# Optimization experiments

Measured on AMD Instinct MI355X. Metric: run time of the kernel, lower is better.

The kernel has to match this reference:

```python
import jax, jax.numpy as jnp
import numpy as np

D_EMBED = 512
NUM_HEADS = 8
HEAD_DIM = D_EMBED // NUM_HEADS
D_FF = 2048
B, L = 2, 4096
LN_EPS = 1e-5


def _layernorm(x, g, b):
    mu = jnp.mean(x, axis=-1, keepdims=True)
    var = jnp.mean(jnp.square(x - mu), axis=-1, keepdims=True)
    return (x - mu) * jax.lax.rsqrt(var + LN_EPS) * g + b


def setup_inputs() -> dict:
    key = jax.random.key(0)
    ks = jax.random.split(key, 16)
    s = 0.02
    inp = {
        "x": jax.random.normal(ks[0], (B, L, D_EMBED), dtype=jnp.float32),
        "mask": jnp.ones((B, 1, 1, L), dtype=jnp.int32),
        # attention projections (stored [in, out] for x @ W)
        "Wq": jax.random.normal(ks[1], (D_EMBED, D_EMBED), dtype=jnp.float32) * s,
        "bq": jnp.zeros((D_EMBED,), dtype=jnp.float32),
        "Wk": jax.random.normal(ks[2], (D_EMBED, D_EMBED), dtype=jnp.float32) * s,
        "bk": jnp.zeros((D_EMBED,), dtype=jnp.float32),
        "Wv": jax.random.normal(ks[3], (D_EMBED, D_EMBED), dtype=jnp.float32) * s,
        "bv": jnp.zeros((D_EMBED,), dtype=jnp.float32),
        "Wo": jax.random.normal(ks[4], (D_EMBED, D_EMBED), dtype=jnp.float32) * s,
        "bo": jnp.zeros((D_EMBED,), dtype=jnp.float32),
        # layernorms
        "ln1_g": jnp.ones((D_EMBED,), dtype=jnp.float32),
        "ln1_b": jnp.zeros((D_EMBED,), dtype=jnp.float32),
        "ln2_g": jnp.ones((D_EMBED,), dtype=jnp.float32),
        "ln2_b": jnp.zeros((D_EMBED,), dtype=jnp.float32),
        # FFN
        "W1": jax.random.normal(ks[5], (D_EMBED, D_FF), dtype=jnp.float32) * s,
        "b1": jnp.zeros((D_FF,), dtype=jnp.float32),
        "W2": jax.random.normal(ks[6], (D_FF, D_EMBED), dtype=jnp.float32) * s,
        "b2": jnp.zeros((D_EMBED,), dtype=jnp.float32),
    }
    return inp


def reference(x, mask, Wq, bq, Wk, bk, Wv, bv, Wo, bo, ln1_g, ln1_b,
              W1, b1, W2, b2, ln2_g, ln2_b):
    Bx, Lx, _ = x.shape
    # projections -> [B, H, L, Dh]
    def split_heads(t):
        return t.reshape(Bx, Lx, NUM_HEADS, HEAD_DIM).transpose(0, 2, 1, 3)
    q = split_heads(x @ Wq + bq)
    k = split_heads(x @ Wk + bk)
    v = split_heads(x @ Wv + bv)
    scores = jnp.einsum("bhqd,bhkd->bhqk", q, k) / jnp.sqrt(
        jnp.asarray(HEAD_DIM, dtype=x.dtype))
    scores = jnp.where(mask == 0, jnp.asarray(-1e9, dtype=x.dtype), scores)
    attn = jax.nn.softmax(scores, axis=-1)
    ctx = jnp.einsum("bhqk,bhkd->bhqd", attn, v)
    ctx = ctx.transpose(0, 2, 1, 3).reshape(Bx, Lx, D_EMBED)
    attn_out = ctx @ Wo + bo

    h = _layernorm(x + attn_out, ln1_g, ln1_b)
    ff = (jax.nn.gelu(h @ W1 + b1, approximate=False)) @ W2 + b2
    return _layernorm(h + ff, ln2_g, ln2_b)
```

## Files before the change

kernel.cpp:

```cpp
#include <hip/hip_runtime.h>
#include <hip/hip_bf16.h>
#include <math.h>

#define D_EMBED 512
#define NUM_HEADS 8
#define HEAD_DIM 64
#define D_FF 2048
#define BATCH 2
#define SEQ 4096
#define M_ROWS (BATCH*SEQ)
#define QSCALE 0.18033688011112042f

typedef __attribute__((ext_vector_type(8))) short short8;
typedef __attribute__((ext_vector_type(4))) short short4_t;
typedef __attribute__((ext_vector_type(4))) float f32x4;
typedef __attribute__((ext_vector_type(16))) float f32x16;

#if __has_builtin(__builtin_amdgcn_exp2f)
#define EXP2(x) __builtin_amdgcn_exp2f(x)
#else
#define EXP2(x) exp2f(x)
#endif

__device__ inline unsigned short f2b(float f) {
    union { float f; unsigned u; } v; v.f = f;
    unsigned r = v.u + 0x7fffu + ((v.u >> 16) & 1u);
    return (unsigned short)(r >> 16);
}

__device__ inline float b2f(short s) {
    union { unsigned u; float f; } v;
    v.u = ((unsigned)(unsigned short)s) << 16;
    return v.f;
}

__device__ inline short4_t pk4(float p0, float p1, float p2, float p3) {
    union { __hip_bfloat162 h2[2]; short4_t s4; } u;
    u.h2[0] = __float22bfloat162_rn(make_float2(p0, p1));
    u.h2[1] = __float22bfloat162_rn(make_float2(p2, p3));
    return u.s4;
}

__device__ inline unsigned pk2(float lo, float hi) {
    union { __hip_bfloat162 h2; unsigned u; } x;
    x.h2 = __float22bfloat162_rn(make_float2(lo, hi));
    return x.u;
}

__device__ inline void plswap(unsigned a, unsigned b, unsigned &r0, unsigned &r1) {
#if __has_builtin(__builtin_amdgcn_permlane32_swap)
    auto v = __builtin_amdgcn_permlane32_swap(a, b, false, false);
    r0 = (unsigned)v[0]; r1 = (unsigned)v[1];
#else
    unsigned ax = (unsigned)__shfl_xor((int)a, 32, 64);
    unsigned bx = (unsigned)__shfl_xor((int)b, 32, 64);
    bool hi = (threadIdx.x & 32) != 0;
    r0 = hi ? bx : a;
    r1 = hi ? b  : ax;
#endif
}

__device__ inline short8 pfrag8(const float* p) {
    unsigned a0 = pk2(p[0], p[1]), a1 = pk2(p[2], p[3]);
    unsigned b0 = pk2(p[4], p[5]), b1 = pk2(p[6], p[7]);
    unsigned u0, u1, u2, u3;
    plswap(a0, b0, u0, u1);
    plswap(a1, b1, u2, u3);
    union { unsigned u[4]; short8 s; } r;
    r.u[0] = u0; r.u[1] = u2; r.u[2] = u1; r.u[3] = u3;
    return r.s;
}

__device__ inline void gl2lds16(const void* g, void* l) {
    __builtin_amdgcn_global_load_lds(
        (const __attribute__((address_space(1))) unsigned int*)g,
        (__attribute__((address_space(3))) unsigned int*)l, 16, 0, 0);
}

template<int EPI>
__global__ __launch_bounds__(256) void gemm_bt(
    const unsigned short* __restrict__ A, const unsigned short* __restrict__ BT,
    const float* __restrict__ bias, void* __restrict__ Cout,
    int M, int N, int K)
{
    __shared__ __align__(16) unsigned short As[128*32];
    __shared__ __align__(16) unsigned short Bs[128*32];
    const int tid  = threadIdx.x;
    const int wave = tid >> 6, lane = tid & 63;
    const int wy = wave >> 1, wx = wave & 1;
    const int quad = lane >> 4, m16 = lane & 15;
    const int row0 = blockIdx.y * 128, n0 = blockIdx.x * 128;
    const int rdoff = (quad ^ ((m16 >> 1) & 3)) * 8;

    f32x4 acc[4][4];
#pragma unroll
    for (int i = 0; i < 4; i++)
#pragma unroll
        for (int j = 0; j < 4; j++) acc[i][j] = (f32x4){0.f,0.f,0.f,0.f};

    const int kIters = K >> 5;
    for (int kt = 0; kt < kIters; ++kt) {
        const int k0 = kt << 5;
#pragma unroll
        for (int it = 0; it < 2; ++it) {
            int g  = it*256 + tid;
            int r  = g >> 2;
            int c8 = (((g & 3) ^ ((g >> 3) & 3)) << 3);
            gl2lds16(A  + (size_t)(row0 + r)*K + k0 + c8, &As[(size_t)(it*256 + wave*64)*8]);
            gl2lds16(BT + (size_t)(n0  + r)*K + k0 + c8, &Bs[(size_t)(it*256 + wave*64)*8]);
        }
        __syncthreads();
        short8 a[4], b[4];
#pragma unroll
        for (int i = 0; i < 4; i++) a[i] = *(const short8*)&As[(wy*64 + i*16 + m16)*32 + rdoff];
#pragma unroll
        for (int j = 0; j < 4; j++) b[j] = *(const short8*)&Bs[(wx*64 + j*16 + m16)*32 + rdoff];
#pragma unroll
        for (int i = 0; i < 4; i++)
#pragma unroll
            for (int j = 0; j < 4; j++)
                acc[i][j] = __builtin_amdgcn_mfma_f32_16x16x32_bf16(a[i], b[j], acc[i][j], 0, 0, 0);
        __syncthreads();
    }

#pragma unroll
    for (int j = 0; j < 4; j++) {
        int col = n0 + wx*64 + j*16 + m16;
        float bj = bias[col];
#pragma unroll
        for (int i = 0; i < 4; i++) {
            int rbase = row0 + wy*64 + i*16 + quad*4;
#pragma unroll
            for (int r = 0; r < 4; r++) {
                float v = acc[i][j][r] + bj;
                size_t idx = (size_t)(rbase + r)*N + col;
                if (EPI == 0) {
                    ((unsigned short*)Cout)[idx] = f2b(v);
                } else {
                    float gv = 0.5f * v * (1.0f + erff(v * 0.70710678118654752f));
                    ((unsigned short*)Cout)[idx] = f2b(gv);
                }
            }
        }
    }
}

__global__ __launch_bounds__(256) void gemm_qkv(
    const unsigned short* __restrict__ A, const unsigned short* __restrict__ BT,
    const float* __restrict__ bias,
    unsigned short* __restrict__ Qp, unsigned short* __restrict__ Kp,
    unsigned short* __restrict__ Vp)
{
    const int K = 512;
    __shared__ __align__(16) unsigned short As[128*32];
    __shared__ __align__(16) unsigned short Bs[128*32];
    const int tid  = threadIdx.x;
    const int wave = tid >> 6, lane = tid & 63;
    const int wy = wave >> 1, wx = wave & 1;
    const int quad = lane >> 4, m16 = lane & 15;
    const int row0 = blockIdx.y * 128, n0 = blockIdx.x * 128;
    const int rdoff = (quad ^ ((m16 >> 1) & 3)) * 8;
    const int region = n0 >> 9;

    f32x4 acc[4][4];
#pragma unroll
    for (int i = 0; i < 4; i++)
#pragma unroll
        for (int j = 0; j < 4; j++) acc[i][j] = (f32x4){0.f,0.f,0.f,0.f};

    for (int kt = 0; kt < 16; ++kt) {
        const int k0 = kt << 5;
#pragma unroll
        for (int it = 0; it < 2; ++it) {
            int g  = it*256 + tid;
            int r  = g >> 2;
            int c8 = (((g & 3) ^ ((g >> 3) & 3)) << 3);
            gl2lds16(A  + (size_t)(row0 + r)*K + k0 + c8, &As[(size_t)(it*256 + wave*64)*8]);
            gl2lds16(BT + (size_t)(n0  + r)*K + k0 + c8, &Bs[(size_t)(it*256 + wave*64)*8]);
        }
        __syncthreads();
        short8 a[4], b[4];
#pragma unroll
        for (int i = 0; i < 4; i++) a[i] = *(const short8*)&As[(wy*64 + i*16 + m16)*32 + rdoff];
#pragma unroll
        for (int j = 0; j < 4; j++) b[j] = *(const short8*)&Bs[(wx*64 + j*16 + m16)*32 + rdoff];
#pragma unroll
        for (int i = 0; i < 4; i++)
#pragma unroll
            for (int j = 0; j < 4; j++)
                acc[i][j] = __builtin_amdgcn_mfma_f32_16x16x32_bf16(a[i], b[j], acc[i][j], 0, 0, 0);
        __syncthreads();
    }

    const float sc = (region == 0) ? QSCALE : 1.0f;
#pragma unroll
    for (int j = 0; j < 4; j++) {
        int col = n0 + wx*64 + j*16 + m16;
        float bj = bias[col];
        int cc = col & 511, h = cc >> 6, d = cc & 63;
#pragma unroll
        for (int i = 0; i < 4; i++) {
            int rbase = row0 + wy*64 + i*16 + quad*4;
#pragma unroll
            for (int r = 0; r < 4; r++) {
                float v = (acc[i][j][r] + bj) * sc;
                int row = rbase + r;
                int b = row >> 12, l = row & 4095;
                size_t bh = (size_t)(b*8 + h);
                if (region == 0) {
                    Qp[(bh*SEQ + l)*64 + d] = f2b(v);
                } else if (region == 1) {
                    Kp[(bh*SEQ + l)*64 + d] = f2b(v);
                } else {
                    Vp[(bh*64 + d)*SEQ + l] = f2b(v);
                }
            }
        }
    }
}

__global__ __launch_bounds__(256) void gemm_bt64(
    const unsigned short* __restrict__ A, const unsigned short* __restrict__ BT,
    const float* __restrict__ bias, unsigned short* __restrict__ Cout,
    int M, int N, int K)
{
    __shared__ __align__(16) unsigned short As[64*32];
    __shared__ __align__(16) unsigned short Bs[128*32];
    const int tid  = threadIdx.x;
    const int wave = tid >> 6, lane = tid & 63;
    const int wy = wave >> 1, wx = wave & 1;
    const int quad = lane >> 4, m16 = lane & 15;
    const int row0 = blockIdx.y * 64, n0 = blockIdx.x * 128;
    const int rdoff = (quad ^ ((m16 >> 1) & 3)) * 8;

    f32x4 acc[2][4];
#pragma unroll
    for (int i = 0; i < 2; i++)
#pragma unroll
        for (int j = 0; j < 4; j++) acc[i][j] = (f32x4){0.f,0.f,0.f,0.f};

    const int kIters = K >> 5;
    for (int kt = 0; kt < kIters; ++kt) {
        const int k0 = kt << 5;
        {
            int r = tid >> 2;
            int c8 = (((tid & 3) ^ ((tid >> 3) & 3)) << 3);
            gl2lds16(A + (size_t)(row0 + r)*K + k0 + c8, &As[(size_t)(wave*64)*8]);
        }
#pragma unroll
        for (int it = 0; it < 2; ++it) {
            int g  = it*256 + tid;
            int r  = g >> 2;
            int c8 = (((g & 3) ^ ((g >> 3) & 3)) << 3);
            gl2lds16(BT + (size_t)(n0 + r)*K + k0 + c8, &Bs[(size_t)(it*256 + wave*64)*8]);
        }
        __syncthreads();
        short8 a[2], b[4];
#pragma unroll
        for (int i = 0; i < 2; i++) a[i] = *(const short8*)&As[(wy*32 + i*16 + m16)*32 + rdoff];
#pragma unroll
        for (int j = 0; j < 4; j++) b[j] = *(const short8*)&Bs[(wx*64 + j*16 + m16)*32 + rdoff];
#pragma unroll
        for (int i = 0; i < 2; i++)
#pragma unroll
            for (int j = 0; j < 4; j++)
                acc[i][j] = __builtin_amdgcn_mfma_f32_16x16x32_bf16(a[i], b[j], acc[i][j], 0, 0, 0);
        __syncthreads();
    }

#pragma unroll
    for (int j = 0; j < 4; j++) {
        int col = n0 + wx*64 + j*16 + m16;
        float bj = bias[col];
#pragma unroll
        for (int i = 0; i < 2; i++) {
            int rbase = row0 + wy*32 + i*16 + quad*4;
#pragma unroll
            for (int r = 0; r < 4; r++) {
                float v = acc[i][j][r] + bj;
                Cout[(size_t)(rbase + r)*N + col] = f2b(v);
            }
        }
    }
}

__global__ __launch_bounds__(256) void prep(
    const float* __restrict__ Wq, const float* __restrict__ Wk,
    const float* __restrict__ Wv, const float* __restrict__ Wo,
    const float* __restrict__ W1, const float* __restrict__ W2,
    const float* __restrict__ bq, const float* __restrict__ bk,
    const float* __restrict__ bv, const int* __restrict__ mask,
    unsigned short* __restrict__ WqkvT, unsigned short* __restrict__ WoT,
    unsigned short* __restrict__ W1T, unsigned short* __restrict__ W2T,
    float* __restrict__ bqkv, int* __restrict__ mflag, unsigned* __restrict__ kmax2)
{
    const int id = blockIdx.x, t = threadIdx.x;
    if (id == 3072) {
        if (t < 64) {
            const int* m = mask + t*128;
            int all = 1;
            for (int i = 0; i < 128; i += 4) {
                int4 v = *(const int4*)(m + i);
                all &= (v.x && v.y && v.z && v.w) ? 1 : 0;
            }
            mflag[t] = all;
        }
        if (t < 16) kmax2[t] = 0u;
        for (int i = t; i < 1536; i += 256)
            bqkv[i] = (i < 512) ? bq[i] : ((i < 1024) ? bk[i-512] : bv[i-1024]);
        return;
    }
    __shared__ float tt[32][33];
    const float* W; unsigned short* WT; int K, N, bx, by;
    if (id < 256)       { W = Wq; WT = WqkvT;            K = 512;  N = 512;  bx = id & 15;  by = id >> 4; }
    else if (id < 512)  { int l = id - 256;  W = Wk; WT = WqkvT + 512*512;  K = 512;  N = 512;  bx = l & 15; by = l >> 4; }
    else if (id < 768)  { int l = id - 512;  W = Wv; WT = WqkvT + 1024*512; K = 512;  N = 512;  bx = l & 15; by = l >> 4; }
    else if (id < 1024) { int l = id - 768;  W = Wo; WT = WoT;              K = 512;  N = 512;  bx = l & 15; by = l >> 4; }
    else if (id < 2048) { int l = id - 1024; W = W1; WT = W1T;              K = 512;  N = 2048; bx = l & 63; by = l >> 6; }
    else                { int l = id - 2048; W = W2; WT = W2T;              K = 2048; N = 512;  bx = l & 15; by = l >> 4; }
    const int n0 = bx*32, k0 = by*32;
    const int x = t & 31, y = t >> 5;
#pragma unroll
    for (int yy = y; yy < 32; yy += 8) tt[yy][x] = W[(size_t)(k0+yy)*N + n0 + x];
    __syncthreads();
#pragma unroll
    for (int yy = y; yy < 32; yy += 8) WT[(size_t)(n0+yy)*K + k0 + x] = f2b(tt[x][yy]);
}

__global__ __launch_bounds__(256) void kmax_k(
    const unsigned short* __restrict__ Kp, unsigned* __restrict__ kmax2)
{
    const int bh = blockIdx.x, t = threadIdx.x;
    const int row = blockIdx.y*256 + t;
    const unsigned short* kp = Kp + ((size_t)bh*SEQ + row)*64;
    float s = 0.f;
#pragma unroll
    for (int c = 0; c < 8; ++c) {
        short8 v = *(const short8*)(kp + c*8);
#pragma unroll
        for (int j = 0; j < 8; ++j) { float f = b2f(v[j]); s += f*f; }
    }
#pragma unroll
    for (int off = 32; off >= 1; off >>= 1)
        s = fmaxf(s, __shfl_xor(s, off, 64));
    if ((t & 63) == 0) atomicMax(&kmax2[bh], __float_as_uint(s));
}

__global__ __launch_bounds__(256, 1) void flash_attn(
    const unsigned short* __restrict__ Qp, const unsigned short* __restrict__ Kp,
    const unsigned short* __restrict__ Vt, const int* __restrict__ mask,
    const int* __restrict__ flags, const unsigned* __restrict__ kmax2,
    unsigned short* __restrict__ O)
{
    __shared__ __align__(16) unsigned short Ks[2][128*64];
    __shared__ __align__(16) unsigned short Vs[2][64*128];
    const int tid = threadIdx.x, wave = tid >> 6, lane = tid & 63;
    const int c = lane & 31, l5 = lane >> 5;
    const int bh = blockIdx.y, b = bh >> 3, h = bh & 7;
    const int qbase = blockIdx.x * 256 + wave * 64;

    const unsigned short* Qb = Qp + (size_t)bh*SEQ*64;
    const unsigned short* Kb = Kp + (size_t)bh*SEQ*64;
    const unsigned short* Vb = Vt + (size_t)bh*64*SEQ;
    const int* mbase = mask + b*SEQ;
    const int* fbase = flags + b*(SEQ/128);
    const float kmx = __uint_as_float(kmax2[bh]);

    short8 qf[2][4];
    float Mq[2];
#pragma unroll
    for (int qs = 0; qs < 2; ++qs) {
        const unsigned short* qp = Qb + (size_t)(qbase + qs*32 + c)*64 + l5*8;
        float qn2 = 0.f;
#pragma unroll
        for (int t = 0; t < 4; ++t) {
            qf[qs][t] = *(const short8*)(qp + t*16);
#pragma unroll
            for (int j = 0; j < 8; ++j) { float f = b2f(qf[qs][t][j]); qn2 += f*f; }
        }
        qn2 += __shfl_xor(qn2, 32, 64);
        Mq[qs] = sqrtf(qn2 * kmx);
    }

    f32x16 accO[2][2];
#pragma unroll
    for (int qs = 0; qs < 2; ++qs)
#pragma unroll
        for (int dg = 0; dg < 2; ++dg)
#pragma unroll
            for (int r = 0; r < 16; ++r) accO[qs][dg][r] = 0.f;
    float rs0 = 0.f, rs1 = 0.f;

#define STAGE(nb, ktn) do {                                                   \
        const int key0s = (ktn)*128;                                          \
        _Pragma("unroll")                                                     \
        for (int it = 0; it < 4; ++it) {                                      \
            int idx = it*256 + tid;                                           \
            int r = idx >> 3, chn = idx & 7;                                  \
            gl2lds16(Kb + (size_t)(key0s + r)*64 + ((chn ^ (r & 7)) << 3),    \
                     &Ks[nb][(it*256 + wave*64)*8]);                          \
        }                                                                     \
        _Pragma("unroll")                                                     \
        for (int it = 0; it < 4; ++it) {                                      \
            int idx = it*256 + tid;                                           \
            int r = idx >> 4, chn = idx & 15;                                 \
            gl2lds16(Vb + (size_t)r*SEQ + key0s + ((chn ^ (r & 15)) << 3),    \
                     &Vs[nb][(it*256 + wave*64)*8]);                          \
        }                                                                     \
    } while (0)

    STAGE(0, 0);
    __syncthreads();
    int cb = 0;

    for (int kt = 0; kt < SEQ/128; ++kt) {
        if (kt + 1 < SEQ/128) STAGE(cb ^ 1, kt + 1);
        const int allones = fbase[kt];
        const int key0 = kt * 128;
        const unsigned short* Kt  = Ks[cb];
        const unsigned short* Vtl = Vs[cb];

#pragma unroll
        for (int kg = 0; kg < 4; ++kg) {
            short8 kf[4];
#pragma unroll
            for (int t = 0; t < 4; ++t) {
                int row = kg*32 + c;
                int chn = (t*2 + l5) ^ (row & 7);
                kf[t] = *(const short8*)&Kt[row*64 + chn*8];
            }
            f32x16 s0, s1;
#pragma unroll
            for (int r = 0; r < 16; ++r) { s0[r] = -Mq[0]; s1[r] = -Mq[1]; }
#pragma unroll
            for (int t = 0; t < 4; ++t) {
                s0 = __builtin_amdgcn_mfma_f32_32x32x16_bf16(kf[t], qf[0][t], s0, 0, 0, 0);
                s1 = __builtin_amdgcn_mfma_f32_32x32x16_bf16(kf[t], qf[1][t], s1, 0, 0, 0);
            }
            if (!allones) {
#pragma unroll
                for (int r = 0; r < 16; ++r) {
                    int mv = mbase[key0 + kg*32 + (r & 3) + 8*(r >> 2) + 4*l5];
                    if (!mv) { s0[r] = -1e9f; s1[r] = -1e9f; }
                }
            }
            float pa[16], pc[16];
#pragma unroll
            for (int r = 0; r < 16; ++r) { pa[r] = EXP2(s0[r]); pc[r] = EXP2(s1[r]); }
            rs0 += (((pa[0]+pa[1])+(pa[2]+pa[3])) + ((pa[4]+pa[5])+(pa[6]+pa[7])))
                 + (((pa[8]+pa[9])+(pa[10]+pa[11])) + ((pa[12]+pa[13])+(pa[14]+pa[15])));
            rs1 += (((pc[0]+pc[1])+(pc[2]+pc[3])) + ((pc[4]+pc[5])+(pc[6]+pc[7])))
                 + (((pc[8]+pc[9])+(pc[10]+pc[11])) + ((pc[12]+pc[13])+(pc[14]+pc[15])));

            short8 vf[2][2];
#pragma unroll
            for (int c2 = 0; c2 < 2; ++c2)
#pragma unroll
                for (int dg = 0; dg < 2; ++dg) {
                    int row = dg*32 + c;
                    int chn = ((kg*2 + c2)*2 + l5) ^ (row & 15);
                    vf[c2][dg] = *(const short8*)&Vtl[row*128 + chn*8];
                }
#pragma unroll
            for (int c2 = 0; c2 < 2; ++c2) {
                short8 pf0 = pfrag8(&pa[c2*8]);
                short8 pf1 = pfrag8(&pc[c2*8]);
                accO[0][0] = __builtin_amdgcn_mfma_f32_32x32x16_bf16(vf[c2][0], pf0, accO[0][0], 0, 0, 0);
                accO[0][1] = __builtin_amdgcn_mfma_f32_32x32x16_bf16(vf[c2][1], pf0, accO[0][1], 0, 0, 0);
                accO[1][0] = __builtin_amdgcn_mfma_f32_32x32x16_bf16(vf[c2][0], pf1, accO[1][0], 0, 0, 0);
                accO[1][1] = __builtin_amdgcn_mfma_f32_32x32x16_bf16(vf[c2][1], pf1, accO[1][1], 0, 0, 0);
            }
        }
        __syncthreads();
        cb ^= 1;
    }
#undef STAGE

    rs0 += __shfl_xor(rs0, 32, 64);
    rs1 += __shfl_xor(rs1, 32, 64);
    float rl[2] = { 1.0f/rs0, 1.0f/rs1 };
#pragma unroll
    for (int qs = 0; qs < 2; ++qs) {
        int qrow = qbase + qs*32 + c;
        unsigned short* op = O + (size_t)(b*SEQ + qrow)*D_EMBED + h*HEAD_DIM;
#pragma unroll
        for (int dg = 0; dg < 2; ++dg)
#pragma unroll
            for (int q4 = 0; q4 < 4; ++q4) {
                short4_t o = pk4(accO[qs][dg][q4*4+0]*rl[qs], accO[qs][dg][q4*4+1]*rl[qs],
                                 accO[qs][dg][q4*4+2]*rl[qs], accO[qs][dg][q4*4+3]*rl[qs]);
                *(short4_t*)&op[dg*32 + q4*8 + l5*4] = o;
            }
    }
}

__global__ __launch_bounds__(256) void ln_res1(
    const float* __restrict__ A, const unsigned short* __restrict__ Bv,
    const float* __restrict__ g, const float* __restrict__ be,
    unsigned short* __restrict__ Yb)
{
    const int wave = threadIdx.x >> 6, lane = threadIdx.x & 63;
    const int row = blockIdx.x * 4 + wave;
    const float* ap = A + (size_t)row*512 + lane*8;
    short8 bv = *(const short8*)(Bv + (size_t)row*512 + lane*8);
    float v[8]; float s = 0.f;
#pragma unroll
    for (int j = 0; j < 8; j++) { v[j] = ap[j] + b2f(bv[j]); s += v[j]; }
#pragma unroll
    for (int off = 32; off >= 1; off >>= 1) s += __shfl_xor(s, off, 64);
    float mu = s * (1.f/512.f);
    float q = 0.f;
#pragma unroll
    for (int j = 0; j < 8; j++) { v[j] -= mu; q += v[j]*v[j]; }
#pragma unroll
    for (int off = 32; off >= 1; off >>= 1) q += __shfl_xor(q, off, 64);
    float rstd = rsqrtf(q * (1.f/512.f) + 1e-5f);
#pragma unroll
    for (int j = 0; j < 8; j++) {
        float y = v[j]*rstd*g[lane*8+j] + be[lane*8+j];
        Yb[(size_t)row*512 + lane*8 + j] = f2b(y);
    }
}

__global__ __launch_bounds__(256) void ln_res2(
    const unsigned short* __restrict__ A, const unsigned short* __restrict__ Bv,
    const float* __restrict__ g, const float* __restrict__ be,
    float* __restrict__ Yf)
{
    const int wave = threadIdx.x >> 6, lane = threadIdx.x & 63;
    const int row = blockIdx.x * 4 + wave;
    short8 av = *(const short8*)(A  + (size_t)row*512 + lane*8);
    short8 bv = *(const short8*)(Bv + (size_t)row*512 + lane*8);
    float v[8]; float s = 0.f;
#pragma unroll
    for (int j = 0; j < 8; j++) { v[j] = b2f(av[j]) + b2f(bv[j]); s += v[j]; }
#pragma unroll
    for (int off = 32; off >= 1; off >>= 1) s += __shfl_xor(s, off, 64);
    float mu = s * (1.f/512.f);
    float q = 0.f;
#pragma unroll
    for (int j = 0; j < 8; j++) { v[j] -= mu; q += v[j]*v[j]; }
#pragma unroll
    for (int off = 32; off >= 1; off >>= 1) q += __shfl_xor(q, off, 64);
    float rstd = rsqrtf(q * (1.f/512.f) + 1e-5f);
#pragma unroll
    for (int j = 0; j < 8; j++) {
        float y = v[j]*rstd*g[lane*8+j] + be[lane*8+j];
        Yf[(size_t)row*512 + lane*8 + j] = y;
    }
}

__global__ __launch_bounds__(256) void cvt_f32_bf16(
    const float* __restrict__ X, unsigned short* __restrict__ Y, int n)
{
    int idx = (blockIdx.x * 256 + threadIdx.x) * 4;
    if (idx < n) {
        float4 v = *(const float4*)(X + idx);
        Y[idx+0] = f2b(v.x); Y[idx+1] = f2b(v.y);
        Y[idx+2] = f2b(v.z); Y[idx+3] = f2b(v.w);
    }
}

extern "C" void kernel_launch(void* const* d_in, const int* in_sizes, int n_in,
                              void* d_out, int out_size, void* d_ws, size_t ws_size,
                              hipStream_t stream)
{
    const float* x    = (const float*)d_in[0];
    const int*   mask = (const int*)  d_in[1];
    const float* Wq = (const float*)d_in[2];  const float* bq = (const float*)d_in[3];
    const float* Wk = (const float*)d_in[4];  const float* bk = (const float*)d_in[5];
    const float* Wv = (const float*)d_in[6];  const float* bv = (const float*)d_in[7];
    const float* Wo = (const float*)d_in[8];  const float* bo = (const float*)d_in[9];
    const float* ln1g = (const float*)d_in[10]; const float* ln1b = (const float*)d_in[11];
    const float* ln2g = (const float*)d_in[12]; const float* ln2b = (const float*)d_in[13];
    const float* W1 = (const float*)d_in[14]; const float* b1 = (const float*)d_in[15];
    const float* W2 = (const float*)d_in[16]; const float* b2 = (const float*)d_in[17];
    float* out = (float*)d_out;

    char* ws = (char*)d_ws;
    const size_t MB = 1024*1024;
    unsigned short* xb    = (unsigned short*)(ws + 0);
    unsigned short* WqkvT = (unsigned short*)(ws + 8*MB);
    unsigned short* W1T   = (unsigned short*)(ws + 10*MB);
    unsigned short* W2T   = (unsigned short*)(ws + 12*MB);
    unsigned short* WoT   = (unsigned short*)(ws + 14*MB);
    float*          bqkv  = (float*)(ws + 14*MB + 512*1024);
    int*            mflag = (int*)(ws + 14*MB + 768*1024);
    unsigned*       kmaxb = (unsigned*)(ws + 14*MB + 772*1024);
    unsigned short* Qp    = (unsigned short*)(ws + 15*MB);
    unsigned short* Kp    = (unsigned short*)(ws + 23*MB);
    unsigned short* Vp    = (unsigned short*)(ws + 31*MB);
    unsigned short* ctx   = (unsigned short*)(ws + 39*MB);
    unsigned short* atfb  = (unsigned short*)(ws + 47*MB);
    unsigned short* hb    = (unsigned short*)(ws + 0);
    unsigned short* Gb    = (unsigned short*)(ws + 15*MB);
    unsigned short* ffb   = (unsigned short*)(ws + 47*MB);

    cvt_f32_bf16<<<4096, 256, 0, stream>>>(x, xb, M_ROWS*D_EMBED);
    prep<<<3073, 256, 0, stream>>>(Wq, Wk, Wv, Wo, W1, W2, bq, bk, bv, mask,
                                   WqkvT, WoT, W1T, W2T, bqkv, mflag, kmaxb);

    gemm_qkv<<<dim3(12,64), 256, 0, stream>>>(xb, WqkvT, bqkv, Qp, Kp, Vp);

    kmax_k<<<dim3(16,16), 256, 0, stream>>>(Kp, kmaxb);
    flash_attn<<<dim3(SEQ/256, 16), 256, 0, stream>>>(Qp, Kp, Vp, mask, mflag, kmaxb, ctx);

    gemm_bt64<<<dim3(4,128), 256, 0, stream>>>(ctx, WoT, bo, atfb, M_ROWS, 512, 512);
    ln_res1<<<M_ROWS/4, 256, 0, stream>>>(x, atfb, ln1g, ln1b, hb);

    gemm_bt<2><<<dim3(16,64), 256, 0, stream>>>(hb, W1T, b1, Gb, M_ROWS, D_FF, 512);
    gemm_bt64<<<dim3(4,128), 256, 0, stream>>>(Gb, W2T, b2, ffb, M_ROWS, 512, D_FF);
    ln_res2<<<M_ROWS/4, 256, 0, stream>>>(hb, ffb, ln2g, ln2b, out);
}
```

Baseline: 373.7 us.

## Split flash attention key groups across two wave sets and reduce via LDS

Doubles the flash attention block to 512 threads. Two wave groups share each query tile, and each group processes half of the key sub-groups in every 128-key tile. At the end, the partial output accumulators and row sums from the second group are written to shared memory and added by the first group before normalisation and store. The aim is more waves per CU to hide latency when the grid holds only about one block per CU. In exchange it adds an LDS reduction, and the new launch bounds tighten register limits.

After: 346.1 us. 1.08x faster.

```diff
diff --git a/kernel.cpp b/kernel.cpp
--- a/kernel.cpp
+++ b/kernel.cpp
@@ -346,7 +346,7 @@
     if ((t & 63) == 0) atomicMax(&kmax2[bh], __float_as_uint(s));
 }
 
-__global__ __launch_bounds__(256, 1) void flash_attn(
+__global__ __launch_bounds__(512, 2) void flash_attn(
     const unsigned short* __restrict__ Qp, const unsigned short* __restrict__ Kp,
     const unsigned short* __restrict__ Vt, const int* __restrict__ mask,
     const int* __restrict__ flags, const unsigned* __restrict__ kmax2,
@@ -354,10 +354,12 @@
 {
     __shared__ __align__(16) unsigned short Ks[2][128*64];
     __shared__ __align__(16) unsigned short Vs[2][64*128];
+    __shared__ float rsh[4][2][64];
     const int tid = threadIdx.x, wave = tid >> 6, lane = tid & 63;
+    const int qsub = wave & 3, parity = wave >> 2;
     const int c = lane & 31, l5 = lane >> 5;
     const int bh = blockIdx.y, b = bh >> 3, h = bh & 7;
-    const int qbase = blockIdx.x * 256 + wave * 64;
+    const int qbase = blockIdx.x * 256 + qsub * 64;
 
     const unsigned short* Qb = Qp + (size_t)bh*SEQ*64;
     const unsigned short* Kb = Kp + (size_t)bh*SEQ*64;
@@ -394,34 +396,36 @@
 #define STAGE(nb, ktn) do {                                                   \
         const int key0s = (ktn)*128;                                          \
         _Pragma("unroll")                                                     \
-        for (int it = 0; it < 4; ++it) {                                      \
-            int idx = it*256 + tid;                                           \
+        for (int it = 0; it < 2; ++it) {                                      \
+            int idx = it*512 + tid;                                           \
             int r = idx >> 3, chn = idx & 7;                                  \
             gl2lds16(Kb + (size_t)(key0s + r)*64 + ((chn ^ (r & 7)) << 3),    \
-                     &Ks[nb][(it*256 + wave*64)*8]);                          \
+                     &Ks[nb][(it*512 + wave*64)*8]);                          \
         }                                                                     \
         _Pragma("unroll")                                                     \
-        for (int it = 0; it < 4; ++it) {                                      \
-            int idx = it*256 + tid;                                           \
+        for (int it = 0; it < 2; ++it) {                                      \
+            int idx = it*512 + tid;                                           \
             int r = idx >> 4, chn = idx & 15;                                 \
             gl2lds16(Vb + (size_t)r*SEQ + key0s + ((chn ^ (r & 15)) << 3),    \
-                     &Vs[nb][(it*256 + wave*64)*8]);                          \
+                     &Vs[nb][(it*512 + wave*64)*8]);                          \
         }                                                                     \
     } while (0)
 
     STAGE(0, 0);
     __syncthreads();
     int cb = 0;
-
-    for (int kt = 0; kt < SEQ/128; ++kt) {
-        if (kt + 1 < SEQ/128) STAGE(cb ^ 1, kt + 1);
+    const int NT = SEQ/128;
+
+    for (int kt = 0; kt < NT; ++kt) {
+        if (kt + 1 < NT) STAGE(cb ^ 1, kt + 1);
         const int allones = fbase[kt];
         const int key0 = kt * 128;
         const unsigned short* Kt  = Ks[cb];
         const unsigned short* Vtl = Vs[cb];
 
 #pragma unroll
-        for (int kg = 0; kg < 4; ++kg) {
+        for (int g = 0; g < 2; ++g) {
+            const int kg = parity*2 + g;
             short8 kf[4];
 #pragma unroll
             for (int t = 0; t < 4; ++t) {
@@ -476,21 +480,47 @@
     }
 #undef STAGE
 
-    rs0 += __shfl_xor(rs0, 32, 64);
-    rs1 += __shfl_xor(rs1, 32, 64);
-    float rl[2] = { 1.0f/rs0, 1.0f/rs1 };
-#pragma unroll
-    for (int qs = 0; qs < 2; ++qs) {
-        int qrow = qbase + qs*32 + c;
-        unsigned short* op = O + (size_t)(b*SEQ + qrow)*D_EMBED + h*HEAD_DIM;
-#pragma unroll
-        for (int dg = 0; dg < 2; ++dg)
-#pragma unroll
-            for (int q4 = 0; q4 < 4; ++q4) {
-                short4_t o = pk4(accO[qs][dg][q4*4+0]*rl[qs], accO[qs][dg][q4*4+1]*rl[qs],
-                                 accO[qs][dg][q4*4+2]*rl[qs], accO[qs][dg][q4*4+3]*rl[qs]);
-                *(short4_t*)&op[dg*32 + q4*8 + l5*4] = o;
-            }
+    float* mp = (qsub < 2) ? ((float*)&Ks[0][0] + qsub*4096)
+                           : ((float*)&Vs[0][0] + (qsub - 2)*4096);
+    if (parity) {
+#pragma unroll
+        for (int qs = 0; qs < 2; ++qs)
+#pragma unroll
+            for (int dg = 0; dg < 2; ++dg)
+#pragma unroll
+                for (int r = 0; r < 16; ++r)
+                    mp[(qs*2 + dg)*1024 + r*64 + lane] = accO[qs][dg][r];
+        rsh[qsub][0][lane] = rs0;
+        rsh[qsub][1][lane] = rs1;
+    }
+    __syncthreads();
+    if (!parity) {
+#pragma unroll
+        for (int qs = 0; qs < 2; ++qs)
+#pragma unroll
+            for (int dg = 0; dg < 2; ++dg)
+#pragma unroll
+                for (int r = 0; r < 16; ++r)
+                    accO[qs][dg][r] += mp[(qs*2 + dg)*1024 + r*64 + lane];
+        rs0 += rsh[qsub][0][lane];
+        rs1 += rsh[qsub][1][lane];
+
+        rs0 += __shfl_xor(rs0, 32, 64);
+        rs1 += __shfl_xor(rs1, 32, 64);
+        float rl[2] = { 1.0f/rs0, 1.0f/rs1 };
+#pragma unroll
+        for (int qs = 0; qs < 2; ++qs) {
+            int qrow = qbase + qs*32 + c;
+            unsigned short* op = O + (size_t)(b*SEQ + qrow)*D_EMBED + h*HEAD_DIM;
+#pragma unroll
+            for (int dg = 0; dg < 2; ++dg)
+#pragma unroll
+                for (int q4 = 0; q4 < 4; ++q4) {
+                    short4_t o = pk4(accO[qs][dg][q4*4+0]*rl[qs], accO[qs][dg][q4*4+1]*rl[qs],
+                                     accO[qs][dg][q4*4+2]*rl[qs], accO[qs][dg][q4*4+3]*rl[qs]);
+                    *(short4_t*)&op[dg*32 + q4*8 + l5*4] = o;
+                }
+        }
     }
 }
 
@@ -603,7 +633,7 @@
     gemm_qkv<<<dim3(12,64), 256, 0, stream>>>(xb, WqkvT, bqkv, Qp, Kp, Vp);
 
     kmax_k<<<dim3(16,16), 256, 0, stream>>>(Kp, kmaxb);
-    flash_attn<<<dim3(SEQ/256, 16), 256, 0, stream>>>(Qp, Kp, Vp, mask, mflag, kmaxb, ctx);
+    flash_attn<<<dim3(SEQ/256, 16), 512, 0, stream>>>(Qp, Kp, Vp, mask, mflag, kmaxb, ctx);
 
     gemm_bt64<<<dim3(4,128), 256, 0, stream>>>(ctx, WoT, bo, atfb, M_ROWS, 512, 512);
     ln_res1<<<M_ROWS/4, 256, 0, stream>>>(x, atfb, ln1g, ln1b, hb);
```
